# Kernel optimization log

Hardware: AMD Instinct MI355X
Metric: run time of the kernel (lower is better)

The kernel has to match this reference:

```python
import jax, jax.numpy as jnp
import numpy as np
import math

B, SQ, SK = 8, 1024, 1024
DIM_Q = DIM_K = DIM_V = 512
H = 8
EPS = 1e-5
INF = jnp.float32(1e38)


def _ln(x, g, b):
    mu = jnp.mean(x, axis=-1, keepdims=True)
    var = jnp.mean(jnp.square(x - mu), axis=-1, keepdims=True)
    return (x - mu) * jax.lax.rsqrt(var + EPS) * g + b


def setup_inputs() -> dict:
    key = jax.random.key(0)
    ks = jax.random.split(key, 12)
    s = 1.0 / math.sqrt(DIM_V)
    return {
        "queries": jax.random.normal(ks[0], (B, SQ, DIM_Q), jnp.float32),
        "keys": jax.random.normal(ks[1], (B, SK, DIM_K), jnp.float32),
        # binary presence masks (as in the original usage)
        "presence_q": (jax.random.uniform(ks[2], (B, SQ)) > 0.1).astype(jnp.float32),
        "presence_k": (jax.random.uniform(ks[3], (B, SK)) > 0.1).astype(jnp.float32),
        "num_heads": H,
        "Wq": jax.random.normal(ks[4], (DIM_Q, DIM_V), jnp.float32) * s,
        "bq": jnp.zeros((DIM_V,), jnp.float32),
        "Wk": jax.random.normal(ks[5], (DIM_K, DIM_V), jnp.float32) * s,
        "bk": jnp.zeros((DIM_V,), jnp.float32),
        "Wv": jax.random.normal(ks[6], (DIM_K, DIM_V), jnp.float32) * s,
        "bv": jnp.zeros((DIM_V,), jnp.float32),
        "Wo": jax.random.normal(ks[7], (DIM_V, DIM_V), jnp.float32) * s,
        "bo": jnp.zeros((DIM_V,), jnp.float32),
        "g0": jnp.ones((DIM_V,), jnp.float32),
        "b0": jnp.zeros((DIM_V,), jnp.float32),
        "g1": jnp.ones((DIM_V,), jnp.float32),
        "b1": jnp.zeros((DIM_V,), jnp.float32),
    }


def reference(queries, keys, presence_q, presence_k, num_heads,
              Wq, bq, Wk, bk, Wv, bv, Wo, bo, g0, b0, g1, b1):
    b, sq, _ = queries.shape
    dim_v = Wq.shape[1]
    d = dim_v // num_heads
    q = queries @ Wq + bq                              # [B,Sq,V]
    k = keys @ Wk + bk                                 # [B,Sk,V]
    v = keys @ Wv + bv                                 # [B,Sk,V]
    qh = q.reshape(b, sq, num_heads, d)
    kh = k.reshape(b, -1, num_heads, d)
    vh = v.reshape(b, -1, num_heads, d)
    logits = jnp.einsum('bqhd,bkhd->bhqk', qh, kh) / jnp.float32(math.sqrt(dim_v))
    pq = presence_q[:, None, :, None]                  # [B,1,Sq,1]
    logits = pq * logits - (1.0 - pq) * INF
    pk = presence_k[:, None, None, :]                  # [B,1,1,Sk]
    logits = pk * logits - (1.0 - pk) * INF
    A = jax.nn.softmax(logits, axis=-1)                # [B,H,Sq,Sk]
    o = qh + jnp.einsum('bhqk,bkhd->bqhd', A, vh)      # residual add of Q_
    o = o.reshape(b, sq, dim_v)
    o = _ln(o, g0, b0)
    o = o + jax.nn.relu(o @ Wo + bo)
    o = _ln(o, g1, b1)
    return o
```

## Files before the change

kernel.cpp:

```cpp
#include <hip/hip_runtime.h>

typedef __attribute__((ext_vector_type(8))) short short8;
typedef __attribute__((ext_vector_type(4))) float f32x4;

#define SCALE2 0.06375871571f

__device__ __forceinline__ float bfu(unsigned short u){
  return __uint_as_float(((unsigned int)u) << 16);
}
__device__ __forceinline__ unsigned short f2b(float x){
  unsigned int b = __float_as_uint(x);
  return (unsigned short)((b + 0x7fffu + ((b>>16)&1u)) >> 16);
}
__device__ __forceinline__ uint4 pack8(const float* f){
  float4 a = *(const float4*)f, b = *(const float4*)(f+4);
  uint4 r;
  r.x = (unsigned)f2b(a.x) | ((unsigned)f2b(a.y)<<16);
  r.y = (unsigned)f2b(a.z) | ((unsigned)f2b(a.w)<<16);
  r.z = (unsigned)f2b(b.x) | ((unsigned)f2b(b.y)<<16);
  r.w = (unsigned)f2b(b.z) | ((unsigned)f2b(b.w)<<16);
  return r;
}

__global__ __launch_bounds__(256) void prep_inputs(
    const float* Wq, const float* Wk, const float* Wv, const float* Wo,
    const float* q, const float* k, unsigned short* wt, unsigned short* qk_dst)
{
  const int id = blockIdx.x, t = threadIdx.x;
  if (id < 256){
    const int m = id >> 6;
    const float* W = (m==0)?Wq:(m==1)?Wk:(m==2)?Wv:Wo;
    unsigned short* dst = wt + (long)m*262144;
    __shared__ unsigned short tile[64][72];
    const int n0 = ((id>>3)&7)*64, k0 = (id&7)*64;
    {
      int r = t>>2, c0 = (t&3)*16;
      uint4 u0 = pack8(W + (long)(k0+r)*512 + n0 + c0);
      uint4 u1 = pack8(W + (long)(k0+r)*512 + n0 + c0 + 8);
      unsigned short* us0 = (unsigned short*)&u0;
      unsigned short* us1 = (unsigned short*)&u1;
      #pragma unroll
      for (int i=0;i<8;++i) tile[c0+i][r] = us0[i];
      #pragma unroll
      for (int i=0;i<8;++i) tile[c0+8+i][r] = us1[i];
    }
    __syncthreads();
    {
      int n = t>>2, ks = (t&3)*16;
      *(uint4*)(dst + (long)(n0+n)*512 + k0 + ks)     = *(uint4*)&tile[n][ks];
      *(uint4*)(dst + (long)(n0+n)*512 + k0 + ks + 8) = *(uint4*)&tile[n][ks+8];
    }
  } else {
    long i = ((long)(id-256)*256 + t)*8;
    const float* src = (i < 4194304) ? q + i : k + (i - 4194304);
    *(uint4*)(qk_dst + i) = pack8(src);
  }
}

__global__ __launch_bounds__(256) void proj_mfma(
    const unsigned short* qin, const unsigned short* kin, const unsigned short* wt,
    const float* bq, const float* bk, const float* bv,
    unsigned short* q_bf, unsigned short* k_bf, unsigned short* vt_bf)
{
  const int mat = blockIdx.z;
  const unsigned short* A = (mat==0)? qin : kin;
  const unsigned short* Wt = wt + (long)mat*262144;
  const float* bias = (mat==0)?bq:(mat==1)?bk:bv;
  const int row0 = blockIdx.y*128, col0 = blockIdx.x*128;
  __shared__ unsigned short As[2][128][40];
  __shared__ unsigned short Ws[2][128][40];
  const int t = threadIdx.x;
  const int lane = t & 63, wid = t >> 6;
  const int ln = lane & 15, quad = lane >> 4;
  const int wy = wid >> 1, wx = wid & 1;
  f32x4 acc[4][4];
  #pragma unroll
  for (int i=0;i<4;++i){
    #pragma unroll
    for (int j=0;j<4;++j) acc[i][j] = (f32x4){0.f,0.f,0.f,0.f};
  }
  const int sr = t>>1, sk0 = (t&1)*16;
  const unsigned short* Arow = A  + (long)(row0+sr)*512 + sk0;
  const unsigned short* Wrow = Wt + (long)(col0+sr)*512 + sk0;
  uint4 a0 = *(const uint4*)(Arow);
  uint4 a1 = *(const uint4*)(Arow + 8);
  uint4 w0 = *(const uint4*)(Wrow);
  uint4 w1 = *(const uint4*)(Wrow + 8);
  *(uint4*)&As[0][sr][sk0]   = a0;
  *(uint4*)&As[0][sr][sk0+8] = a1;
  *(uint4*)&Ws[0][sr][sk0]   = w0;
  *(uint4*)&Ws[0][sr][sk0+8] = w1;
  __syncthreads();
  for (int it=0; it<16; ++it){
    const int cur = it & 1;
    if (it < 15){
      a0 = *(const uint4*)(Arow + (it+1)*32);
      a1 = *(const uint4*)(Arow + (it+1)*32 + 8);
      w0 = *(const uint4*)(Wrow + (it+1)*32);
      w1 = *(const uint4*)(Wrow + (it+1)*32 + 8);
    }
    short8 a[4], b[4];
    #pragma unroll
    for (int mt=0;mt<4;++mt) a[mt] = *(const short8*)&As[cur][wy*64+mt*16+ln][quad*8];
    #pragma unroll
    for (int nt=0;nt<4;++nt) b[nt] = *(const short8*)&Ws[cur][wx*64+nt*16+ln][quad*8];
    #pragma unroll
    for (int mt=0;mt<4;++mt){
      #pragma unroll
      for (int nt=0;nt<4;++nt)
        acc[mt][nt] = __builtin_amdgcn_mfma_f32_16x16x32_bf16(a[mt], b[nt], acc[mt][nt], 0,0,0);
    }
    if (it < 15){
      *(uint4*)&As[cur^1][sr][sk0]   = a0;
      *(uint4*)&As[cur^1][sr][sk0+8] = a1;
      *(uint4*)&Ws[cur^1][sr][sk0]   = w0;
      *(uint4*)&Ws[cur^1][sr][sk0+8] = w1;
    }
    __syncthreads();
  }
  float bias_v[4];
  #pragma unroll
  for (int nt=0;nt<4;++nt) bias_v[nt] = bias[col0 + wx*64 + nt*16 + ln];
  if (mat < 2){
    unsigned short* dst = (mat==0)? q_bf : k_bf;
    #pragma unroll
    for (int mt=0;mt<4;++mt){
      int row = row0 + wy*64 + mt*16 + quad*4;
      #pragma unroll
      for (int nt=0;nt<4;++nt){
        int col = col0 + wx*64 + nt*16 + ln;
        #pragma unroll
        for (int r=0;r<4;++r)
          dst[(long)(row+r)*512 + col] = f2b(acc[mt][nt][r] + bias_v[nt]);
      }
    }
  } else {
    #pragma unroll
    for (int mt=0;mt<4;++mt){
      int row = row0 + wy*64 + mt*16 + quad*4;
      int bb = row >> 10, sk = row & 1023;
      #pragma unroll
      for (int nt=0;nt<4;++nt){
        int col = col0 + wx*64 + nt*16 + ln;
        int h = col >> 6, dd = col & 63;
        uint2 pk2; unsigned short* pp = (unsigned short*)&pk2;
        #pragma unroll
        for (int r=0;r<4;++r) pp[r] = f2b(acc[mt][nt][r] + bias_v[nt]);
        *(uint2*)(vt_bf + (((long)((bb*8+h)*64+dd)) << 10) + sk) = pk2;
      }
    }
  }
}

__global__ __launch_bounds__(256) void attn_mfma(
    const unsigned short* q_bf, const unsigned short* k_bf, const unsigned short* vt_bf,
    const float* pres_q, const float* pres_k, unsigned short* o_bf)
{
  const int bx = blockIdx.x;
  const int b = bx >> 3, h = bx & 7;
  const int q0 = blockIdx.y * 128;
  const int t = threadIdx.x;
  const int lane = t & 63, wid = t >> 6, ln = lane & 15, quad = lane >> 4;
  __shared__ unsigned short QP[128][72];
  __shared__ unsigned short Ks[2][64][72];
  __shared__ unsigned short Vt[2][64][72];
  __shared__ float pq_s[128];
  __shared__ float pk_s[2][64];
  {
    int tok = t>>1, ds = (t&1)*32;
    const unsigned short* src = q_bf + (long)(b*1024 + q0 + tok)*512 + h*64 + ds;
    *(uint4*)&QP[tok][ds]    = *(const uint4*)src;
    *(uint4*)&QP[tok][ds+8]  = *(const uint4*)(src+8);
    *(uint4*)&QP[tok][ds+16] = *(const uint4*)(src+16);
    *(uint4*)&QP[tok][ds+24] = *(const uint4*)(src+24);
  }
  {
    int tok = t>>2, ds = (t&3)*16;
    const unsigned short* sk = k_bf + (long)(b*1024 + tok)*512 + h*64 + ds;
    *(uint4*)&Ks[0][tok][ds]   = *(const uint4*)sk;
    *(uint4*)&Ks[0][tok][ds+8] = *(const uint4*)(sk+8);
    const unsigned short* sv = vt_bf + (((long)((b*8+h)*64 + tok)) << 10) + ds;
    *(uint4*)&Vt[0][tok][ds]   = *(const uint4*)sv;
    *(uint4*)&Vt[0][tok][ds+8] = *(const uint4*)(sv+8);
  }
  if (t < 128) pq_s[t] = pres_q[b*1024 + q0 + t];
  if (t < 64)  pk_s[0][t] = pres_k[b*1024 + t];
  __syncthreads();
  short8 aq[2][2];
  float av[2][4], mval[2][4];
  #pragma unroll
  for (int s=0;s<2;++s){
    aq[s][0] = *(const short8*)&QP[wid*32+s*16+ln][quad*8];
    aq[s][1] = *(const short8*)&QP[wid*32+s*16+ln][32+quad*8];
    #pragma unroll
    for (int r=0;r<4;++r){
      av[s][r] = pq_s[wid*32 + s*16 + quad*4 + r]*SCALE2;
      mval[s][r] = (av[s][r] == 0.f) ? 0.f : -43.f;
    }
  }
  f32x4 oacc[2][4];
  float lsum[2][4];
  #pragma unroll
  for (int s=0;s<2;++s){
    #pragma unroll
    for (int i=0;i<4;++i){ oacc[s][i] = (f32x4){0.f,0.f,0.f,0.f}; lsum[s][i] = 0.f; }
  }

  for (int it=0; it<16; ++it){
    const int cur = it & 1;
    const int k0n = (it+1)*64;
    uint4 pf_k0, pf_k1, pf_v0, pf_v1; float pf_p = 0.f;
    if (it < 15){
      int tok = t>>2, ds = (t&3)*16;
      const unsigned short* sk = k_bf + (long)(b*1024 + k0n + tok)*512 + h*64 + ds;
      pf_k0 = *(const uint4*)sk;
      pf_k1 = *(const uint4*)(sk+8);
      const unsigned short* sv = vt_bf + (((long)((b*8+h)*64 + tok)) << 10) + k0n + ds;
      pf_v0 = *(const uint4*)sv;
      pf_v1 = *(const uint4*)(sv+8);
      if (t < 64) pf_p = pres_k[b*1024 + k0n + t];
    }
    f32x4 s[2][4];
    #pragma unroll
    for (int st=0;st<2;++st){
      #pragma unroll
      for (int kt=0;kt<4;++kt) s[st][kt] = (f32x4){0.f,0.f,0.f,0.f};
    }
    #pragma unroll
    for (int kt=0;kt<4;++kt){
      short8 kb0 = *(const short8*)&Ks[cur][kt*16+ln][quad*8];
      short8 kb1 = *(const short8*)&Ks[cur][kt*16+ln][32+quad*8];
      #pragma unroll
      for (int st=0;st<2;++st){
        s[st][kt] = __builtin_amdgcn_mfma_f32_16x16x32_bf16(aq[st][0], kb0, s[st][kt], 0,0,0);
        s[st][kt] = __builtin_amdgcn_mfma_f32_16x16x32_bf16(aq[st][1], kb1, s[st][kt], 0,0,0);
      }
    }
    float pk4[4];
    #pragma unroll
    for (int kt=0;kt<4;++kt) pk4[kt] = pk_s[cur][kt*16+ln];
    #pragma unroll
    for (int st=0;st<2;++st){
      #pragma unroll
      for (int r=0;r<4;++r){
        #pragma unroll
        for (int kt=0;kt<4;++kt){
          float x0 = s[st][kt][r]*av[st][r];
          float x = __builtin_fmaf(pk4[kt], x0 - mval[st][r], mval[st][r]);
          float e = __builtin_amdgcn_exp2f(x);
          lsum[st][r] += e;
          QP[wid*32+st*16+quad*4+r][kt*16+ln] = (unsigned short)(__float_as_uint(e) >> 16);
        }
      }
    }
    short8 ap[2][2];
    #pragma unroll
    for (int st=0;st<2;++st){
      ap[st][0] = *(const short8*)&QP[wid*32+st*16+ln][quad*8];
      ap[st][1] = *(const short8*)&QP[wid*32+st*16+ln][32+quad*8];
    }
    #pragma unroll
    for (int dt=0;dt<4;++dt){
      short8 vb0 = *(const short8*)&Vt[cur][dt*16+ln][quad*8];
      short8 vb1 = *(const short8*)&Vt[cur][dt*16+ln][32+quad*8];
      #pragma unroll
      for (int st=0;st<2;++st){
        oacc[st][dt] = __builtin_amdgcn_mfma_f32_16x16x32_bf16(ap[st][0], vb0, oacc[st][dt], 0,0,0);
        oacc[st][dt] = __builtin_amdgcn_mfma_f32_16x16x32_bf16(ap[st][1], vb1, oacc[st][dt], 0,0,0);
      }
    }
    if (it < 15){
      int tok = t>>2, ds = (t&3)*16;
      *(uint4*)&Ks[cur^1][tok][ds]   = pf_k0;
      *(uint4*)&Ks[cur^1][tok][ds+8] = pf_k1;
      *(uint4*)&Vt[cur^1][tok][ds]   = pf_v0;
      *(uint4*)&Vt[cur^1][tok][ds+8] = pf_v1;
      if (t < 64) pk_s[cur^1][t] = pf_p;
    }
    __syncthreads();
  }
  #pragma unroll
  for (int st=0;st<2;++st){
    #pragma unroll
    for (int r=0;r<4;++r){
      float l = lsum[st][r];
      #pragma unroll
      for (int msk=1; msk<16; msk<<=1) l += __shfl_xor(l, msk);
      float inv = 1.f / l;
      int ql = wid*32 + st*16 + quad*4 + r;
      long base = (long)(b*1024 + q0 + ql)*512 + h*64;
      #pragma unroll
      for (int dt=0;dt<4;++dt){
        float qh = bfu(q_bf[base + dt*16 + ln]);
        o_bf[base + dt*16 + ln] = f2b(qh + oacc[st][dt][r]*inv);
      }
    }
  }
}

__global__ __launch_bounds__(256) void ln_kernel(
    const unsigned short* in, void* outp, int mode, const float* g, const float* bvec)
{
  const int row = blockIdx.x*4 + (threadIdx.x >> 6);
  const int lane = threadIdx.x & 63;
  uint4 raw = *(const uint4*)(in + (long)row*512 + lane*8);
  const unsigned short* rs16 = (const unsigned short*)&raw;
  float v[8];
  #pragma unroll
  for (int c=0;c<8;++c) v[c] = bfu(rs16[c]);
  float sum = 0.f;
  #pragma unroll
  for (int c=0;c<8;++c) sum += v[c];
  #pragma unroll
  for (int msk=1; msk<64; msk<<=1) sum += __shfl_xor(sum, msk);
  float mu = sum * (1.f/512.f);
  float var = 0.f;
  #pragma unroll
  for (int c=0;c<8;++c){ v[c] -= mu; var += v[c]*v[c]; }
  #pragma unroll
  for (int msk=1; msk<64; msk<<=1) var += __shfl_xor(var, msk);
  float rs = rsqrtf(var*(1.f/512.f) + 1e-5f);
  float gv[8], bv[8];
  *(float4*)&gv[0] = *(const float4*)(g + lane*8);
  *(float4*)&gv[4] = *(const float4*)(g + lane*8 + 4);
  *(float4*)&bv[0] = *(const float4*)(bvec + lane*8);
  *(float4*)&bv[4] = *(const float4*)(bvec + lane*8 + 4);
  float y[8];
  #pragma unroll
  for (int c=0;c<8;++c) y[c] = v[c]*rs*gv[c] + bv[c];
  if (mode){
    float* dst = (float*)outp + (long)row*512 + lane*8;
    *(float4*)dst       = *(float4*)&y[0];
    *(float4*)(dst + 4) = *(float4*)&y[4];
  } else {
    uint4 out; unsigned short* os = (unsigned short*)&out;
    #pragma unroll
    for (int c=0;c<8;++c) os[c] = f2b(y[c]);
    *(uint4*)((unsigned short*)outp + (long)row*512 + lane*8) = out;
  }
}

__global__ __launch_bounds__(256) void out_mfma(
    const unsigned short* t_bf, const unsigned short* Wt, const float* bo,
    unsigned short* u_bf)
{
  const int row0 = blockIdx.y*64, col0 = blockIdx.x*128;
  __shared__ unsigned short As[2][64][40];
  __shared__ unsigned short Ws[2][128][40];
  const int t = threadIdx.x;
  const int lane = t & 63, wid = t >> 6;
  const int ln = lane & 15, quad = lane >> 4;
  const int wy = wid >> 1, wx = wid & 1;
  f32x4 acc[2][4];
  #pragma unroll
  for (int i=0;i<2;++i){
    #pragma unroll
    for (int j=0;j<4;++j) acc[i][j] = (f32x4){0.f,0.f,0.f,0.f};
  }
  const int ar = t>>2, ac0 = (t&3)*8;
  const int wr = t>>1, wc0 = (t&1)*16;
  const unsigned short* Arow = t_bf + (long)(row0+ar)*512 + ac0;
  const unsigned short* Wrow = Wt   + (long)(col0+wr)*512 + wc0;
  uint4 a0 = *(const uint4*)(Arow);
  uint4 w0 = *(const uint4*)(Wrow);
  uint4 w1 = *(const uint4*)(Wrow + 8);
  *(uint4*)&As[0][ar][ac0] = a0;
  *(uint4*)&Ws[0][wr][wc0]   = w0;
  *(uint4*)&Ws[0][wr][wc0+8] = w1;
  __syncthreads();
  for (int it=0; it<16; ++it){
    const int cur = it & 1;
    if (it < 15){
      a0 = *(const uint4*)(Arow + (it+1)*32);
      w0 = *(const uint4*)(Wrow + (it+1)*32);
      w1 = *(const uint4*)(Wrow + (it+1)*32 + 8);
    }
    short8 a[2], b[4];
    #pragma unroll
    for (int mt=0;mt<2;++mt) a[mt] = *(const short8*)&As[cur][wy*32+mt*16+ln][quad*8];
    #pragma unroll
    for (int nt=0;nt<4;++nt) b[nt] = *(const short8*)&Ws[cur][wx*64+nt*16+ln][quad*8];
    #pragma unroll
    for (int mt=0;mt<2;++mt){
      #pragma unroll
      for (int nt=0;nt<4;++nt)
        acc[mt][nt] = __builtin_amdgcn_mfma_f32_16x16x32_bf16(a[mt], b[nt], acc[mt][nt], 0,0,0);
    }
    if (it < 15){
      *(uint4*)&As[cur^1][ar][ac0] = a0;
      *(uint4*)&Ws[cur^1][wr][wc0]   = w0;
      *(uint4*)&Ws[cur^1][wr][wc0+8] = w1;
    }
    __syncthreads();
  }
  float bias_v[4];
  #pragma unroll
  for (int nt=0;nt<4;++nt) bias_v[nt] = bo[col0 + wx*64 + nt*16 + ln];
  #pragma unroll
  for (int mt=0;mt<2;++mt){
    int row = row0 + wy*32 + mt*16 + quad*4;
    #pragma unroll
    for (int nt=0;nt<4;++nt){
      int col = col0 + wx*64 + nt*16 + ln;
      #pragma unroll
      for (int r=0;r<4;++r){
        long idx = (long)(row+r)*512 + col;
        float u = acc[mt][nt][r] + bias_v[nt];
        u = fmaxf(u, 0.f);
        u_bf[idx] = f2b(bfu(t_bf[idx]) + u);
      }
    }
  }
}

extern "C" void kernel_launch(void* const* d_in, const int* in_sizes, int n_in,
                              void* d_out, int out_size, void* d_ws, size_t ws_size,
                              hipStream_t stream)
{
  unsigned short* q_bf  = (unsigned short*)d_ws;
  unsigned short* k_bf  = q_bf  + 8192l*512;
  unsigned short* vt_bf = k_bf  + 8192l*512;
  unsigned short* t_bf  = vt_bf + 8192l*512;
  unsigned short* wt    = t_bf  + 8192l*512;
  unsigned short* qin   = wt + 4l*512*512;
  unsigned short* kin   = qin + 4194304;
  unsigned short* o_bf  = qin;
  unsigned short* u_bf  = kin;

  hipLaunchKernelGGL(prep_inputs, dim3(4352), dim3(256), 0, stream,
                     (const float*)d_in[5], (const float*)d_in[7],
                     (const float*)d_in[9], (const float*)d_in[11],
                     (const float*)d_in[0], (const float*)d_in[1], wt, qin);
  hipLaunchKernelGGL(proj_mfma, dim3(4,64,3), dim3(256), 0, stream,
                     qin, kin, wt,
                     (const float*)d_in[6], (const float*)d_in[8],
                     (const float*)d_in[10], q_bf, k_bf, vt_bf);
  hipLaunchKernelGGL(attn_mfma, dim3(64,8), dim3(256), 0, stream,
                     q_bf, k_bf, vt_bf,
                     (const float*)d_in[2], (const float*)d_in[3], o_bf);
  hipLaunchKernelGGL(ln_kernel, dim3(2048), dim3(256), 0, stream,
                     o_bf, (void*)t_bf, 0, (const float*)d_in[13], (const float*)d_in[14]);
  hipLaunchKernelGGL(out_mfma, dim3(4,128), dim3(256), 0, stream,
                     t_bf, wt + 3l*512*512, (const float*)d_in[12], u_bf);
  hipLaunchKernelGGL(ln_kernel, dim3(2048), dim3(256), 0, stream,
                     u_bf, d_out, 1, (const float*)d_in[15], (const float*)d_in[16]);
}
```

Before: 206.0 us.

## Restructure attention to 64-query tiles with transposed S MFMA and per-wave P buffer

Halves the query tile per block (64 instead of 128) and doubles the grid so each wave handles 16 query rows. The score MFMA is computed transposed (K as A operand), which lets each lane do a vectorized softmax over 4 keys with rounded bf16 packing into a small per-wave LDS buffer instead of a 128-row shared Q/P array. It also adds a launch-bounds occupancy hint and s_setprio around the MFMA phases. The aim is to raise occupancy and cut LDS/register pressure, at the cost of reloading K/V tiles for twice as many blocks.

Result: slower. 214.0 us (+3.9%).

```diff
diff --git a/kernel.cpp b/kernel.cpp
--- a/kernel.cpp
+++ b/kernel.cpp
@@ -152,28 +152,19 @@
   }
 }
 
-__global__ __launch_bounds__(256) void attn_mfma(
+__global__ __launch_bounds__(256, 3) void attn_mfma(
     const unsigned short* q_bf, const unsigned short* k_bf, const unsigned short* vt_bf,
     const float* pres_q, const float* pres_k, unsigned short* o_bf)
 {
   const int bx = blockIdx.x;
   const int b = bx >> 3, h = bx & 7;
-  const int q0 = blockIdx.y * 128;
+  const int q0 = blockIdx.y * 64;
   const int t = threadIdx.x;
   const int lane = t & 63, wid = t >> 6, ln = lane & 15, quad = lane >> 4;
-  __shared__ unsigned short QP[128][72];
   __shared__ unsigned short Ks[2][64][72];
   __shared__ unsigned short Vt[2][64][72];
-  __shared__ float pq_s[128];
+  __shared__ unsigned short Pw[4][16][72];
   __shared__ float pk_s[2][64];
-  {
-    int tok = t>>1, ds = (t&1)*32;
-    const unsigned short* src = q_bf + (long)(b*1024 + q0 + tok)*512 + h*64 + ds;
-    *(uint4*)&QP[tok][ds]    = *(const uint4*)src;
-    *(uint4*)&QP[tok][ds+8]  = *(const uint4*)(src+8);
-    *(uint4*)&QP[tok][ds+16] = *(const uint4*)(src+16);
-    *(uint4*)&QP[tok][ds+24] = *(const uint4*)(src+24);
-  }
   {
     int tok = t>>2, ds = (t&3)*16;
     const unsigned short* sk = k_bf + (long)(b*1024 + tok)*512 + h*64 + ds;
@@ -183,28 +174,17 @@
     *(uint4*)&Vt[0][tok][ds]   = *(const uint4*)sv;
     *(uint4*)&Vt[0][tok][ds+8] = *(const uint4*)(sv+8);
   }
-  if (t < 128) pq_s[t] = pres_q[b*1024 + q0 + t];
-  if (t < 64)  pk_s[0][t] = pres_k[b*1024 + t];
+  if (t < 64) pk_s[0][t] = pres_k[b*1024 + t];
+  const unsigned short* qrow = q_bf + (long)(b*1024 + q0 + wid*16 + ln)*512 + h*64;
+  short8 aq0 = *(const short8*)(qrow + quad*8);
+  short8 aq1 = *(const short8*)(qrow + 32 + quad*8);
+  const float av = SCALE2 * pres_q[b*1024 + q0 + wid*16 + ln];
+  const float mval = (av == 0.f) ? 0.f : -43.f;
+  f32x4 oacc[4];
+  #pragma unroll
+  for (int i=0;i<4;++i) oacc[i] = (f32x4){0.f,0.f,0.f,0.f};
+  float lsum = 0.f;
   __syncthreads();
-  short8 aq[2][2];
-  float av[2][4], mval[2][4];
-  #pragma unroll
-  for (int s=0;s<2;++s){
-    aq[s][0] = *(const short8*)&QP[wid*32+s*16+ln][quad*8];
-    aq[s][1] = *(const short8*)&QP[wid*32+s*16+ln][32+quad*8];
-    #pragma unroll
-    for (int r=0;r<4;++r){
-      av[s][r] = pq_s[wid*32 + s*16 + quad*4 + r]*SCALE2;
-      mval[s][r] = (av[s][r] == 0.f) ? 0.f : -43.f;
-    }
-  }
-  f32x4 oacc[2][4];
-  float lsum[2][4];
-  #pragma unroll
-  for (int s=0;s<2;++s){
-    #pragma unroll
-    for (int i=0;i<4;++i){ oacc[s][i] = (f32x4){0.f,0.f,0.f,0.f}; lsum[s][i] = 0.f; }
-  }
 
   for (int it=0; it<16; ++it){
     const int cur = it & 1;
@@ -220,55 +200,46 @@
       pf_v1 = *(const uint4*)(sv+8);
       if (t < 64) pf_p = pres_k[b*1024 + k0n + t];
     }
-    f32x4 s[2][4];
-    #pragma unroll
-    for (int st=0;st<2;++st){
-      #pragma unroll
-      for (int kt=0;kt<4;++kt) s[st][kt] = (f32x4){0.f,0.f,0.f,0.f};
-    }
+    f32x4 sc[4];
+    #pragma unroll
+    for (int kt=0;kt<4;++kt) sc[kt] = (f32x4){0.f,0.f,0.f,0.f};
+    __builtin_amdgcn_s_setprio(1);
     #pragma unroll
     for (int kt=0;kt<4;++kt){
       short8 kb0 = *(const short8*)&Ks[cur][kt*16+ln][quad*8];
       short8 kb1 = *(const short8*)&Ks[cur][kt*16+ln][32+quad*8];
-      #pragma unroll
-      for (int st=0;st<2;++st){
-        s[st][kt] = __builtin_amdgcn_mfma_f32_16x16x32_bf16(aq[st][0], kb0, s[st][kt], 0,0,0);
-        s[st][kt] = __builtin_amdgcn_mfma_f32_16x16x32_bf16(aq[st][1], kb1, s[st][kt], 0,0,0);
-      }
-    }
-    float pk4[4];
-    #pragma unroll
-    for (int kt=0;kt<4;++kt) pk4[kt] = pk_s[cur][kt*16+ln];
-    #pragma unroll
-    for (int st=0;st<2;++st){
-      #pragma unroll
-      for (int r=0;r<4;++r){
-        #pragma unroll
-        for (int kt=0;kt<4;++kt){
-          float x0 = s[st][kt][r]*av[st][r];
-          float x = __builtin_fmaf(pk4[kt], x0 - mval[st][r], mval[st][r]);
-          float e = __builtin_amdgcn_exp2f(x);
-          lsum[st][r] += e;
-          QP[wid*32+st*16+quad*4+r][kt*16+ln] = (unsigned short)(__float_as_uint(e) >> 16);
-        }
-      }
-    }
-    short8 ap[2][2];
-    #pragma unroll
-    for (int st=0;st<2;++st){
-      ap[st][0] = *(const short8*)&QP[wid*32+st*16+ln][quad*8];
-      ap[st][1] = *(const short8*)&QP[wid*32+st*16+ln][32+quad*8];
-    }
+      sc[kt] = __builtin_amdgcn_mfma_f32_16x16x32_bf16(kb0, aq0, sc[kt], 0,0,0);
+      sc[kt] = __builtin_amdgcn_mfma_f32_16x16x32_bf16(kb1, aq1, sc[kt], 0,0,0);
+    }
+    __builtin_amdgcn_s_setprio(0);
+    #pragma unroll
+    for (int kt=0;kt<4;++kt){
+      float4 pk4 = *(const float4*)&pk_s[cur][kt*16 + quad*4];
+      float x0 = __builtin_fmaf(pk4.x, __builtin_fmaf(sc[kt][0], av, -mval), mval);
+      float x1 = __builtin_fmaf(pk4.y, __builtin_fmaf(sc[kt][1], av, -mval), mval);
+      float x2 = __builtin_fmaf(pk4.z, __builtin_fmaf(sc[kt][2], av, -mval), mval);
+      float x3 = __builtin_fmaf(pk4.w, __builtin_fmaf(sc[kt][3], av, -mval), mval);
+      float e0 = __builtin_amdgcn_exp2f(x0);
+      float e1 = __builtin_amdgcn_exp2f(x1);
+      float e2 = __builtin_amdgcn_exp2f(x2);
+      float e3 = __builtin_amdgcn_exp2f(x3);
+      lsum += (e0+e1)+(e2+e3);
+      uint2 w;
+      w.x = (unsigned)f2b(e0) | ((unsigned)f2b(e1)<<16);
+      w.y = (unsigned)f2b(e2) | ((unsigned)f2b(e3)<<16);
+      *(uint2*)&Pw[wid][ln][kt*16 + quad*4] = w;
+    }
+    short8 ap0 = *(const short8*)&Pw[wid][ln][quad*8];
+    short8 ap1 = *(const short8*)&Pw[wid][ln][32 + quad*8];
+    __builtin_amdgcn_s_setprio(1);
     #pragma unroll
     for (int dt=0;dt<4;++dt){
       short8 vb0 = *(const short8*)&Vt[cur][dt*16+ln][quad*8];
       short8 vb1 = *(const short8*)&Vt[cur][dt*16+ln][32+quad*8];
-      #pragma unroll
-      for (int st=0;st<2;++st){
-        oacc[st][dt] = __builtin_amdgcn_mfma_f32_16x16x32_bf16(ap[st][0], vb0, oacc[st][dt], 0,0,0);
-        oacc[st][dt] = __builtin_amdgcn_mfma_f32_16x16x32_bf16(ap[st][1], vb1, oacc[st][dt], 0,0,0);
-      }
-    }
+      oacc[dt] = __builtin_amdgcn_mfma_f32_16x16x32_bf16(ap0, vb0, oacc[dt], 0,0,0);
+      oacc[dt] = __builtin_amdgcn_mfma_f32_16x16x32_bf16(ap1, vb1, oacc[dt], 0,0,0);
+    }
+    __builtin_amdgcn_s_setprio(0);
     if (it < 15){
       int tok = t>>2, ds = (t&3)*16;
       *(uint4*)&Ks[cur^1][tok][ds]   = pf_k0;
@@ -279,21 +250,19 @@
     }
     __syncthreads();
   }
-  #pragma unroll
-  for (int st=0;st<2;++st){
-    #pragma unroll
-    for (int r=0;r<4;++r){
-      float l = lsum[st][r];
-      #pragma unroll
-      for (int msk=1; msk<16; msk<<=1) l += __shfl_xor(l, msk);
-      float inv = 1.f / l;
-      int ql = wid*32 + st*16 + quad*4 + r;
-      long base = (long)(b*1024 + q0 + ql)*512 + h*64;
-      #pragma unroll
-      for (int dt=0;dt<4;++dt){
-        float qh = bfu(q_bf[base + dt*16 + ln]);
-        o_bf[base + dt*16 + ln] = f2b(qh + oacc[st][dt][r]*inv);
-      }
+  float l = lsum;
+  l += __shfl_xor(l, 16);
+  l += __shfl_xor(l, 32);
+  #pragma unroll
+  for (int r=0;r<4;++r){
+    float lr = __shfl(l, quad*4 + r);
+    float inv = 1.f / lr;
+    int ql = wid*16 + quad*4 + r;
+    long base = (long)(b*1024 + q0 + ql)*512 + h*64;
+    #pragma unroll
+    for (int dt=0;dt<4;++dt){
+      float qh = bfu(q_bf[base + dt*16 + ln]);
+      o_bf[base + dt*16 + ln] = f2b(qh + oacc[dt][r]*inv);
     }
   }
 }
@@ -435,7 +404,7 @@
                      qin, kin, wt,
                      (const float*)d_in[6], (const float*)d_in[8],
                      (const float*)d_in[10], q_bf, k_bf, vt_bf);
-  hipLaunchKernelGGL(attn_mfma, dim3(64,8), dim3(256), 0, stream,
+  hipLaunchKernelGGL(attn_mfma, dim3(64,16), dim3(256), 0, stream,
                      q_bf, k_bf, vt_bf,
                      (const float*)d_in[2], (const float*)d_in[3], o_bf);
   hipLaunchKernelGGL(ln_kernel, dim3(2048), dim3(256), 0, stream,
```

## Fuse LN0, output projection and LN1 into one kernel; convert inputs inside projection

Applied to the files above, without the earlier changes.

Fp32-to-bf16 conversion of queries and keys moves out of the prep kernel and into the projection GEMM's tile loads, which removes a full write and re-read of the converted activations. The two layernorm kernels and the output GEMM are merged into a single kernel. Each 512-thread block owns 32 full rows, applies LN0 in shared memory, runs the 512-column GEMM, adds the residual and ReLU, and applies LN1 before writing fp32 output. This drops two launches and several intermediate global round trips. In exchange, the fused kernel runs only 256 blocks with heavy shared-memory use, and every block re-streams all of Wo, so parallelism is lower.

New measurement: 211.1 us. 1.03x slower.

```diff
diff --git a/kernel.cpp b/kernel.cpp
--- a/kernel.cpp
+++ b/kernel.cpp
@@ -22,48 +22,42 @@
   return r;
 }
 
-__global__ __launch_bounds__(256) void prep_inputs(
+__global__ __launch_bounds__(256) void prep_w(
     const float* Wq, const float* Wk, const float* Wv, const float* Wo,
-    const float* q, const float* k, unsigned short* wt, unsigned short* qk_dst)
+    unsigned short* wt)
 {
   const int id = blockIdx.x, t = threadIdx.x;
-  if (id < 256){
-    const int m = id >> 6;
-    const float* W = (m==0)?Wq:(m==1)?Wk:(m==2)?Wv:Wo;
-    unsigned short* dst = wt + (long)m*262144;
-    __shared__ unsigned short tile[64][72];
-    const int n0 = ((id>>3)&7)*64, k0 = (id&7)*64;
-    {
-      int r = t>>2, c0 = (t&3)*16;
-      uint4 u0 = pack8(W + (long)(k0+r)*512 + n0 + c0);
-      uint4 u1 = pack8(W + (long)(k0+r)*512 + n0 + c0 + 8);
-      unsigned short* us0 = (unsigned short*)&u0;
-      unsigned short* us1 = (unsigned short*)&u1;
-      #pragma unroll
-      for (int i=0;i<8;++i) tile[c0+i][r] = us0[i];
-      #pragma unroll
-      for (int i=0;i<8;++i) tile[c0+8+i][r] = us1[i];
-    }
-    __syncthreads();
-    {
-      int n = t>>2, ks = (t&3)*16;
-      *(uint4*)(dst + (long)(n0+n)*512 + k0 + ks)     = *(uint4*)&tile[n][ks];
-      *(uint4*)(dst + (long)(n0+n)*512 + k0 + ks + 8) = *(uint4*)&tile[n][ks+8];
-    }
-  } else {
-    long i = ((long)(id-256)*256 + t)*8;
-    const float* src = (i < 4194304) ? q + i : k + (i - 4194304);
-    *(uint4*)(qk_dst + i) = pack8(src);
+  const int m = id >> 6;
+  const float* W = (m==0)?Wq:(m==1)?Wk:(m==2)?Wv:Wo;
+  unsigned short* dst = wt + (long)m*262144;
+  __shared__ unsigned short tile[64][72];
+  const int n0 = ((id>>3)&7)*64, k0 = (id&7)*64;
+  {
+    int r = t>>2, c0 = (t&3)*16;
+    uint4 u0 = pack8(W + (long)(k0+r)*512 + n0 + c0);
+    uint4 u1 = pack8(W + (long)(k0+r)*512 + n0 + c0 + 8);
+    unsigned short* us0 = (unsigned short*)&u0;
+    unsigned short* us1 = (unsigned short*)&u1;
+    #pragma unroll
+    for (int i=0;i<8;++i) tile[c0+i][r] = us0[i];
+    #pragma unroll
+    for (int i=0;i<8;++i) tile[c0+8+i][r] = us1[i];
+  }
+  __syncthreads();
+  {
+    int n = t>>2, ks = (t&3)*16;
+    *(uint4*)(dst + (long)(n0+n)*512 + k0 + ks)     = *(uint4*)&tile[n][ks];
+    *(uint4*)(dst + (long)(n0+n)*512 + k0 + ks + 8) = *(uint4*)&tile[n][ks+8];
   }
 }
 
 __global__ __launch_bounds__(256) void proj_mfma(
-    const unsigned short* qin, const unsigned short* kin, const unsigned short* wt,
+    const float* qf, const float* kf, const unsigned short* wt,
     const float* bq, const float* bk, const float* bv,
     unsigned short* q_bf, unsigned short* k_bf, unsigned short* vt_bf)
 {
   const int mat = blockIdx.z;
-  const unsigned short* A = (mat==0)? qin : kin;
+  const float* A = (mat==0)? qf : kf;
   const unsigned short* Wt = wt + (long)mat*262144;
   const float* bias = (mat==0)?bq:(mat==1)?bk:bv;
   const int row0 = blockIdx.y*128, col0 = blockIdx.x*128;
@@ -80,10 +74,10 @@
     for (int j=0;j<4;++j) acc[i][j] = (f32x4){0.f,0.f,0.f,0.f};
   }
   const int sr = t>>1, sk0 = (t&1)*16;
-  const unsigned short* Arow = A  + (long)(row0+sr)*512 + sk0;
+  const float* Arow = A + (long)(row0+sr)*512 + sk0;
   const unsigned short* Wrow = Wt + (long)(col0+sr)*512 + sk0;
-  uint4 a0 = *(const uint4*)(Arow);
-  uint4 a1 = *(const uint4*)(Arow + 8);
+  uint4 a0 = pack8(Arow);
+  uint4 a1 = pack8(Arow + 8);
   uint4 w0 = *(const uint4*)(Wrow);
   uint4 w1 = *(const uint4*)(Wrow + 8);
   *(uint4*)&As[0][sr][sk0]   = a0;
@@ -94,8 +88,8 @@
   for (int it=0; it<16; ++it){
     const int cur = it & 1;
     if (it < 15){
-      a0 = *(const uint4*)(Arow + (it+1)*32);
-      a1 = *(const uint4*)(Arow + (it+1)*32 + 8);
+      a0 = pack8(Arow + (it+1)*32);
+      a1 = pack8(Arow + (it+1)*32 + 8);
       w0 = *(const uint4*)(Wrow + (it+1)*32);
       w1 = *(const uint4*)(Wrow + (it+1)*32 + 8);
     }
@@ -298,88 +292,87 @@
   }
 }
 
-__global__ __launch_bounds__(256) void ln_kernel(
-    const unsigned short* in, void* outp, int mode, const float* g, const float* bvec)
+__global__ __launch_bounds__(512, 2) void out_ln(
+    const unsigned short* o_bf, const unsigned short* Wt, const float* bo,
+    const float* g0, const float* b0, const float* g1, const float* b1,
+    float* out)
 {
-  const int row = blockIdx.x*4 + (threadIdx.x >> 6);
-  const int lane = threadIdx.x & 63;
-  uint4 raw = *(const uint4*)(in + (long)row*512 + lane*8);
-  const unsigned short* rs16 = (const unsigned short*)&raw;
-  float v[8];
-  #pragma unroll
-  for (int c=0;c<8;++c) v[c] = bfu(rs16[c]);
-  float sum = 0.f;
-  #pragma unroll
-  for (int c=0;c<8;++c) sum += v[c];
-  #pragma unroll
-  for (int msk=1; msk<64; msk<<=1) sum += __shfl_xor(sum, msk);
-  float mu = sum * (1.f/512.f);
-  float var = 0.f;
-  #pragma unroll
-  for (int c=0;c<8;++c){ v[c] -= mu; var += v[c]*v[c]; }
-  #pragma unroll
-  for (int msk=1; msk<64; msk<<=1) var += __shfl_xor(var, msk);
-  float rs = rsqrtf(var*(1.f/512.f) + 1e-5f);
-  float gv[8], bv[8];
-  *(float4*)&gv[0] = *(const float4*)(g + lane*8);
-  *(float4*)&gv[4] = *(const float4*)(g + lane*8 + 4);
-  *(float4*)&bv[0] = *(const float4*)(bvec + lane*8);
-  *(float4*)&bv[4] = *(const float4*)(bvec + lane*8 + 4);
-  float y[8];
-  #pragma unroll
-  for (int c=0;c<8;++c) y[c] = v[c]*rs*gv[c] + bv[c];
-  if (mode){
-    float* dst = (float*)outp + (long)row*512 + lane*8;
-    *(float4*)dst       = *(float4*)&y[0];
-    *(float4*)(dst + 4) = *(float4*)&y[4];
-  } else {
-    uint4 out; unsigned short* os = (unsigned short*)&out;
-    #pragma unroll
-    for (int c=0;c<8;++c) os[c] = f2b(y[c]);
-    *(uint4*)((unsigned short*)outp + (long)row*512 + lane*8) = out;
-  }
-}
-
-__global__ __launch_bounds__(256) void out_mfma(
-    const unsigned short* t_bf, const unsigned short* Wt, const float* bo,
-    unsigned short* u_bf)
-{
-  const int row0 = blockIdx.y*64, col0 = blockIdx.x*128;
-  __shared__ unsigned short As[2][64][40];
-  __shared__ unsigned short Ws[2][128][40];
+  const int row0 = blockIdx.x * 32;
   const int t = threadIdx.x;
-  const int lane = t & 63, wid = t >> 6;
-  const int ln = lane & 15, quad = lane >> 4;
-  const int wy = wid >> 1, wx = wid & 1;
+  const int lane = t & 63, wid = t >> 6, ln = lane & 15, quad = lane >> 4;
+
+  __shared__ unsigned short To[32][520];
+  __shared__ unsigned short Ws[2][512][40];
+
+  {
+    int r = t >> 4, c0 = (t & 15) * 32;
+    const unsigned short* src = o_bf + (long)(row0 + r)*512 + c0;
+    #pragma unroll
+    for (int i=0;i<4;++i)
+      *(uint4*)&To[r][c0 + i*8] = *(const uint4*)(src + i*8);
+  }
+  {
+    const unsigned short* wr = Wt + (long)t*512;
+    #pragma unroll
+    for (int i=0;i<4;++i)
+      *(uint4*)&Ws[0][t][i*8] = *(const uint4*)(wr + i*8);
+  }
+  __syncthreads();
+  {
+    float gv[8], bv[8];
+    *(float4*)&gv[0] = *(const float4*)(g0 + lane*8);
+    *(float4*)&gv[4] = *(const float4*)(g0 + lane*8 + 4);
+    *(float4*)&bv[0] = *(const float4*)(b0 + lane*8);
+    *(float4*)&bv[4] = *(const float4*)(b0 + lane*8 + 4);
+    #pragma unroll
+    for (int i=0;i<4;++i){
+      int r = wid*4 + i;
+      uint4 raw = *(const uint4*)&To[r][lane*8];
+      const unsigned short* rs16 = (const unsigned short*)&raw;
+      float v[8];
+      #pragma unroll
+      for (int c=0;c<8;++c) v[c] = bfu(rs16[c]);
+      float sum = 0.f;
+      #pragma unroll
+      for (int c=0;c<8;++c) sum += v[c];
+      #pragma unroll
+      for (int msk=1; msk<64; msk<<=1) sum += __shfl_xor(sum, msk);
+      float mu = sum * (1.f/512.f);
+      float var = 0.f;
+      #pragma unroll
+      for (int c=0;c<8;++c){ v[c] -= mu; var += v[c]*v[c]; }
+      #pragma unroll
+      for (int msk=1; msk<64; msk<<=1) var += __shfl_xor(var, msk);
+      float rs = rsqrtf(var*(1.f/512.f) + 1e-5f);
+      uint4 o4; unsigned short* os = (unsigned short*)&o4;
+      #pragma unroll
+      for (int c=0;c<8;++c) os[c] = f2b(v[c]*rs*gv[c] + bv[c]);
+      *(uint4*)&To[r][lane*8] = o4;
+    }
+  }
+  __syncthreads();
+
   f32x4 acc[2][4];
   #pragma unroll
   for (int i=0;i<2;++i){
     #pragma unroll
     for (int j=0;j<4;++j) acc[i][j] = (f32x4){0.f,0.f,0.f,0.f};
   }
-  const int ar = t>>2, ac0 = (t&3)*8;
-  const int wr = t>>1, wc0 = (t&1)*16;
-  const unsigned short* Arow = t_bf + (long)(row0+ar)*512 + ac0;
-  const unsigned short* Wrow = Wt   + (long)(col0+wr)*512 + wc0;
-  uint4 a0 = *(const uint4*)(Arow);
-  uint4 w0 = *(const uint4*)(Wrow);
-  uint4 w1 = *(const uint4*)(Wrow + 8);
-  *(uint4*)&As[0][ar][ac0] = a0;
-  *(uint4*)&Ws[0][wr][wc0]   = w0;
-  *(uint4*)&Ws[0][wr][wc0+8] = w1;
-  __syncthreads();
   for (int it=0; it<16; ++it){
     const int cur = it & 1;
-    if (it < 15){
-      a0 = *(const uint4*)(Arow + (it+1)*32);
-      w0 = *(const uint4*)(Wrow + (it+1)*32);
-      w1 = *(const uint4*)(Wrow + (it+1)*32 + 8);
+    uint4 pw0, pw1, pw2, pw3;
+    if (it < 15){
+      const unsigned short* wr = Wt + (long)t*512 + (it+1)*32;
+      pw0 = *(const uint4*)(wr);
+      pw1 = *(const uint4*)(wr + 8);
+      pw2 = *(const uint4*)(wr + 16);
+      pw3 = *(const uint4*)(wr + 24);
     }
     short8 a[2], b[4];
-    #pragma unroll
-    for (int mt=0;mt<2;++mt) a[mt] = *(const short8*)&As[cur][wy*32+mt*16+ln][quad*8];
-    #pragma unroll
-    for (int nt=0;nt<4;++nt) b[nt] = *(const short8*)&Ws[cur][wx*64+nt*16+ln][quad*8];
+    a[0] = *(const short8*)&To[ln][it*32 + quad*8];
+    a[1] = *(const short8*)&To[16+ln][it*32 + quad*8];
+    #pragma unroll
+    for (int nt=0;nt<4;++nt) b[nt] = *(const short8*)&Ws[cur][wid*64 + nt*16 + ln][quad*8];
     #pragma unroll
     for (int mt=0;mt<2;++mt){
       #pragma unroll
@@ -387,28 +380,67 @@
         acc[mt][nt] = __builtin_amdgcn_mfma_f32_16x16x32_bf16(a[mt], b[nt], acc[mt][nt], 0,0,0);
     }
     if (it < 15){
-      *(uint4*)&As[cur^1][ar][ac0] = a0;
-      *(uint4*)&Ws[cur^1][wr][wc0]   = w0;
-      *(uint4*)&Ws[cur^1][wr][wc0+8] = w1;
+      *(uint4*)&Ws[cur^1][t][0]  = pw0;
+      *(uint4*)&Ws[cur^1][t][8]  = pw1;
+      *(uint4*)&Ws[cur^1][t][16] = pw2;
+      *(uint4*)&Ws[cur^1][t][24] = pw3;
     }
     __syncthreads();
   }
-  float bias_v[4];
-  #pragma unroll
-  for (int nt=0;nt<4;++nt) bias_v[nt] = bo[col0 + wx*64 + nt*16 + ln];
-  #pragma unroll
-  for (int mt=0;mt<2;++mt){
-    int row = row0 + wy*32 + mt*16 + quad*4;
-    #pragma unroll
-    for (int nt=0;nt<4;++nt){
-      int col = col0 + wx*64 + nt*16 + ln;
-      #pragma unroll
-      for (int r=0;r<4;++r){
-        long idx = (long)(row+r)*512 + col;
-        float u = acc[mt][nt][r] + bias_v[nt];
-        u = fmaxf(u, 0.f);
-        u_bf[idx] = f2b(bfu(t_bf[idx]) + u);
-      }
+
+  unsigned short* Us = &Ws[0][0][0];
+  {
+    float bo_v[4];
+    #pragma unroll
+    for (int nt=0;nt<4;++nt) bo_v[nt] = bo[wid*64 + nt*16 + ln];
+    #pragma unroll
+    for (int mt=0;mt<2;++mt){
+      int row = mt*16 + quad*4;
+      #pragma unroll
+      for (int nt=0;nt<4;++nt){
+        int col = wid*64 + nt*16 + ln;
+        #pragma unroll
+        for (int r=0;r<4;++r){
+          float tv = bfu(To[row+r][col]);
+          float u = tv + fmaxf(acc[mt][nt][r] + bo_v[nt], 0.f);
+          Us[(long)(row+r)*520 + col] = f2b(u);
+        }
+      }
+    }
+  }
+  __syncthreads();
+  {
+    float gv[8], bv[8];
+    *(float4*)&gv[0] = *(const float4*)(g1 + lane*8);
+    *(float4*)&gv[4] = *(const float4*)(g1 + lane*8 + 4);
+    *(float4*)&bv[0] = *(const float4*)(b1 + lane*8);
+    *(float4*)&bv[4] = *(const float4*)(b1 + lane*8 + 4);
+    #pragma unroll
+    for (int i=0;i<4;++i){
+      int r = wid*4 + i;
+      uint4 raw = *(const uint4*)&Us[(long)r*520 + lane*8];
+      const unsigned short* rs16 = (const unsigned short*)&raw;
+      float v[8];
+      #pragma unroll
+      for (int c=0;c<8;++c) v[c] = bfu(rs16[c]);
+      float sum = 0.f;
+      #pragma unroll
+      for (int c=0;c<8;++c) sum += v[c];
+      #pragma unroll
+      for (int msk=1; msk<64; msk<<=1) sum += __shfl_xor(sum, msk);
+      float mu = sum * (1.f/512.f);
+      float var = 0.f;
+      #pragma unroll
+      for (int c=0;c<8;++c){ v[c] -= mu; var += v[c]*v[c]; }
+      #pragma unroll
+      for (int msk=1; msk<64; msk<<=1) var += __shfl_xor(var, msk);
+      float rs = rsqrtf(var*(1.f/512.f) + 1e-5f);
+      float y[8];
+      #pragma unroll
+      for (int c=0;c<8;++c) y[c] = v[c]*rs*gv[c] + bv[c];
+      float* dst = out + (long)(row0 + r)*512 + lane*8;
+      *(float4*)dst       = *(float4*)&y[0];
+      *(float4*)(dst + 4) = *(float4*)&y[4];
     }
   }
 }
@@ -420,28 +452,22 @@
   unsigned short* q_bf  = (unsigned short*)d_ws;
   unsigned short* k_bf  = q_bf  + 8192l*512;
   unsigned short* vt_bf = k_bf  + 8192l*512;
-  unsigned short* t_bf  = vt_bf + 8192l*512;
-  unsigned short* wt    = t_bf  + 8192l*512;
-  unsigned short* qin   = wt + 4l*512*512;
-  unsigned short* kin   = qin + 4194304;
-  unsigned short* o_bf  = qin;
-  unsigned short* u_bf  = kin;
-
-  hipLaunchKernelGGL(prep_inputs, dim3(4352), dim3(256), 0, stream,
+  unsigned short* o_bf  = vt_bf + 8192l*512;
+  unsigned short* wt    = o_bf  + 8192l*512;
+
+  hipLaunchKernelGGL(prep_w, dim3(256), dim3(256), 0, stream,
                      (const float*)d_in[5], (const float*)d_in[7],
-                     (const float*)d_in[9], (const float*)d_in[11],
-                     (const float*)d_in[0], (const float*)d_in[1], wt, qin);
+                     (const float*)d_in[9], (const float*)d_in[11], wt);
   hipLaunchKernelGGL(proj_mfma, dim3(4,64,3), dim3(256), 0, stream,
-                     qin, kin, wt,
+                     (const float*)d_in[0], (const float*)d_in[1], wt,
                      (const float*)d_in[6], (const float*)d_in[8],
                      (const float*)d_in[10], q_bf, k_bf, vt_bf);
   hipLaunchKernelGGL(attn_mfma, dim3(64,8), dim3(256), 0, stream,
                      q_bf, k_bf, vt_bf,
                      (const float*)d_in[2], (const float*)d_in[3], o_bf);
-  hipLaunchKernelGGL(ln_kernel, dim3(2048), dim3(256), 0, stream,
-                     o_bf, (void*)t_bf, 0, (const float*)d_in[13], (const float*)d_in[14]);
-  hipLaunchKernelGGL(out_mfma, dim3(4,128), dim3(256), 0, stream,
-                     t_bf, wt + 3l*512*512, (const float*)d_in[12], u_bf);
-  hipLaunchKernelGGL(ln_kernel, dim3(2048), dim3(256), 0, stream,
-                     u_bf, d_out, 1, (const float*)d_in[15], (const float*)d_in[16]);
-}
+  hipLaunchKernelGGL(out_ln, dim3(256), dim3(512), 0, stream,
+                     o_bf, wt + 3l*512*512, (const float*)d_in[12],
+                     (const float*)d_in[13], (const float*)d_in[14],
+                     (const float*)d_in[15], (const float*)d_in[16],
+                     (float*)d_out);
+}
```
